# Kernel tuning notes

Measured on AMD Instinct MI355X. Metric: run time of the kernel, lower is better.

Reference implementation:

```python
import jax, jax.numpy as jnp
import numpy as np

N, E, D, L, G = 10000, 320000, 256, 5, 128
RWSE, DEG_V = 16, 1001
BN_EPS = 1e-5


def setup_inputs() -> dict:
    key = jax.random.key(0)
    ks = jax.random.split(key, 12)
    s = 1.0 / np.sqrt(D)
    return {
        'feat_id': jax.random.randint(ks[0], (N,), 0, 100000, dtype=jnp.int64 if jax.config.jax_enable_x64 else jnp.int32),
        'edge_index': jax.random.randint(ks[1], (2, E), 0, N),
        'batch_idx': jnp.sort(jax.random.randint(ks[2], (N,), 0, G)),
        'rwse': jax.random.normal(ks[3], (N, RWSE), jnp.float32),
        'in_degrees': jax.random.randint(ks[4], (N,), 0, DEG_V),
        # value_projection: Linear(fixed_input_dim=D -> D); stored as [in, out]
        'w_val': jax.random.normal(ks[5], (D, D), jnp.float32) * s,
        'b_val': jnp.zeros((D,), jnp.float32),
        # rwse_projection: Linear(RWSE -> D)
        'w_rwse': jax.random.normal(ks[6], (RWSE, D), jnp.float32) * (1.0 / np.sqrt(RWSE)),
        'b_rwse': jnp.zeros((D,), jnp.float32),
        # degree_embedding table (clamped to [0, 1000])
        'deg_emb': jax.random.normal(ks[7], (DEG_V, D), jnp.float32) * 0.02,
        # per-layer GIN MLP: Linear-ReLU-Linear, stacked over L layers
        'mlp_w1': jax.random.normal(ks[8], (L, D, D), jnp.float32) * s,
        'mlp_b1': jnp.zeros((L, D), jnp.float32),
        'mlp_w2': jax.random.normal(ks[9], (L, D, D), jnp.float32) * s,
        'mlp_b2': jnp.zeros((L, D), jnp.float32),
        # BatchNorm1d (eval mode: running stats)
        'bn_gamma': jnp.ones((L, D), jnp.float32),
        'bn_beta': jnp.zeros((L, D), jnp.float32),
        'bn_mean': jnp.zeros((L, D), jnp.float32),
        'bn_var': jax.random.uniform(ks[10], (L, D), jnp.float32, 0.5, 1.5),
        # GIN eps per layer
        'eps_gin': jnp.zeros((L,), jnp.float32),
    }


def reference(feat_id, edge_index, batch_idx, rwse, in_degrees,
              w_val, b_val, w_rwse, b_rwse, deg_emb,
              mlp_w1, mlp_b1, mlp_w2, mlp_b2,
              bn_gamma, bn_beta, bn_mean, bn_var, eps_gin):
    # --- node feature embedding ---
    h_id = jnp.remainder(feat_id, D)
    h_one = jax.nn.one_hot(h_id, D, dtype=jnp.float32)            # [N, D]
    h = h_one @ w_val + b_val + rwse @ w_rwse + b_rwse            # value + rwse projections
    deg = jnp.clip(in_degrees, 0, 1000)
    h = h + deg_emb[deg]                                          # degree embedding

    src, dst = edge_index[0], edge_index[1]
    for l in range(L):
        # GIN message passing: sum neighbor features into dst (gather -> scatter-add)
        agg = jax.ops.segment_sum(h[src], dst, num_segments=N)    # [N, D]
        y = agg + (1.0 + eps_gin[l]) * h
        # MLP (Linear-ReLU-Linear)
        y = jax.nn.relu(y @ mlp_w1[l] + mlp_b1[l]) @ mlp_w2[l] + mlp_b2[l]
        # BatchNorm1d (eval: running stats) + ReLU
        y = (y - bn_mean[l]) * (bn_gamma[l] * jax.lax.rsqrt(bn_var[l] + BN_EPS)) + bn_beta[l]
        h = jax.nn.relu(y)

    # --- mean pooling per graph ---
    sums = jax.ops.segment_sum(h, batch_idx, num_segments=G)                     # [G, D]
    cnt = jax.ops.segment_sum(jnp.ones((N, 1), h.dtype), batch_idx, num_segments=G)
    graph_feature = sums / jnp.maximum(cnt, 1.0)
    return graph_feature, h
```

## Files before the change

### kernel.cpp

```cpp
#include <hip/hip_runtime.h>
#include <hip/hip_bf16.h>

#define N_NODES 10000
#define N_EDGES 320000
#define DIM     256
#define HDIM    128
#define N_LAYERS 5
#define N_GRAPHS 128
#define RWSE_K  16

typedef __bf16 bf16_t;
typedef bf16_t bf16x8 __attribute__((ext_vector_type(8)));
typedef float  f32x4  __attribute__((ext_vector_type(4)));

__device__ inline ushort f2bf(float f) {
    union { float f; unsigned u; } v; v.f = f;
    unsigned r = v.u + 0x7fff + ((v.u >> 16) & 1);
    return (ushort)(r >> 16);
}
__device__ inline float bfbits2f(unsigned hi16) {
    union { unsigned u; float f; } v; v.u = hi16;
    return v.f;
}

__global__ __launch_bounds__(256)
void setup_kernel(const int* __restrict__ feat_id,
                  const float* __restrict__ rwse,
                  const int* __restrict__ in_deg,
                  const float* __restrict__ w_val,
                  const float* __restrict__ b_val,
                  const float* __restrict__ w_rwse,
                  const float* __restrict__ b_rwse,
                  const float* __restrict__ deg_emb,
                  ushort* __restrict__ hb_lo, ushort* __restrict__ hb_hi,
                  const int* __restrict__ ei, int* __restrict__ cnt_arr,
                  const float* __restrict__ w1, const float* __restrict__ w2,
                  ushort* __restrict__ wt1, ushort* __restrict__ wt2,
                  const float* __restrict__ gamma, const float* __restrict__ beta,
                  const float* __restrict__ mean, const float* __restrict__ var,
                  const float* __restrict__ b2, float* __restrict__ scale,
                  float* __restrict__ shift) {
    __shared__ float r[RWSE_K];
    __shared__ float t[32][33];
    int b = blockIdx.x;
    int tid = threadIdx.x;
    if (b < N_NODES) {
        int i = b, d = tid;
        if (d < RWSE_K) r[d] = rwse[i * RWSE_K + d];
        __syncthreads();
        int hid = feat_id[i] & (DIM - 1);
        int dg = in_deg[i];
        dg = dg < 0 ? 0 : (dg > 1000 ? 1000 : dg);
        float v = w_val[hid * DIM + d] + b_val[d] + b_rwse[d] + deg_emb[dg * DIM + d];
#pragma unroll
        for (int k = 0; k < RWSE_K; ++k) v += r[k] * w_rwse[k * DIM + d];
        int hh = d >> 7, dl = d & (HDIM - 1);
        (hh ? hb_hi : hb_lo)[i * HDIM + dl] = f2bf(v);
    } else if (b < 11250) {
        int e = (b - N_NODES) * 256 + tid;
        if (e < N_EDGES) atomicAdd(&cnt_arr[ei[N_EDGES + e]], 1);
    } else if (b < 11890) {
        int w_id = b - 11250;
        int l = w_id >> 7;
        int rem = w_id & 127;
        int mat = rem >> 6;
        int tile = rem & 63;
        const float* W  = (mat ? w2  : w1)  + (size_t)l * DIM * DIM;
        ushort*      Wt = (mat ? wt2 : wt1) + (size_t)l * DIM * DIM;
        int k0 = (tile >> 3) * 32, n0 = (tile & 7) * 32;
        int tx = tid & 31, ty = tid >> 5;
#pragma unroll
        for (int j = 0; j < 4; ++j)
            t[ty + j * 8][tx] = W[(k0 + ty + j * 8) * DIM + n0 + tx];
        __syncthreads();
#pragma unroll
        for (int j = 0; j < 4; ++j)
            Wt[(n0 + ty + j * 8) * DIM + k0 + tx] = f2bf(t[tx][ty + j * 8]);
    } else {
        int l = b - 11890;
        int idx = l * DIM + tid;
        float s = gamma[idx] * rsqrtf(var[idx] + 1e-5f);
        scale[idx] = s;
        shift[idx] = beta[idx] + (b2[idx] - mean[idx]) * s;
    }
}

__global__ __launch_bounds__(1024)
void scan_kernel(const int* __restrict__ cnt_arr, int* __restrict__ cur, int n) {
    __shared__ int wsum[16];
    __shared__ int carry_sh;
    int tid = threadIdx.x, wave = tid >> 6, lane = tid & 63;
    if (tid == 0) carry_sh = 0;
    __syncthreads();
    for (int base = 0; base < n; base += 1024) {
        int idx = base + tid;
        int v = (idx < n) ? cnt_arr[idx] : 0;
        int s = v;
#pragma unroll
        for (int off = 1; off < 64; off <<= 1) {
            int t = __shfl_up(s, off, 64);
            if (lane >= off) s += t;
        }
        if (lane == 63) wsum[wave] = s;
        __syncthreads();
        if (wave == 0) {
            int ws = (lane < 16) ? wsum[lane] : 0;
#pragma unroll
            for (int off = 1; off < 16; off <<= 1) {
                int t = __shfl_up(ws, off, 64);
                if (lane >= off) ws += t;
            }
            if (lane < 16) wsum[lane] = ws;
        }
        __syncthreads();
        int excl = s - v + (wave ? wsum[wave - 1] : 0) + carry_sh;
        if (idx < n) cur[idx] = excl;
        __syncthreads();
        if (tid == 0) carry_sh += wsum[15];
        __syncthreads();
    }
}

__global__ __launch_bounds__(256)
void fill_kernel(const int* __restrict__ ei, int* __restrict__ cur,
                 int* __restrict__ cs) {
    int e = blockIdx.x * 256 + threadIdx.x;
    if (e < N_EDGES) {
        int d = ei[N_EDGES + e];
        int p = atomicAdd(&cur[d], 1);
        cs[p] = ei[e];
    }
}

#define ACCV(v)                                                        \
    acc[0] += bfbits2f((v).x << 16); acc[1] += bfbits2f((v).x & 0xffff0000u); \
    acc[2] += bfbits2f((v).y << 16); acc[3] += bfbits2f((v).y & 0xffff0000u); \
    acc[4] += bfbits2f((v).z << 16); acc[5] += bfbits2f((v).z & 0xffff0000u); \
    acc[6] += bfbits2f((v).w << 16); acc[7] += bfbits2f((v).w & 0xffff0000u);

__global__ __launch_bounds__(256)
void agg_kernel(const ushort* __restrict__ hbH,
                const int* __restrict__ cur, const int* __restrict__ cs,
                const float* __restrict__ eps_gin, int layer, int hh,
                ushort* __restrict__ y) {
    int wave = threadIdx.x >> 6;
    int lane = threadIdx.x & 63;
    int quarter = lane >> 4;
    int sl = lane & 15;
    int i = blockIdx.x * 4 + wave;
    if (i >= N_NODES) return;
    const uint4* hb4 = (const uint4*)hbH;
    float acc[8];
#pragma unroll
    for (int t = 0; t < 8; ++t) acc[t] = 0.f;

    int e0 = i ? cur[i - 1] : 0;
    int e1 = cur[i];
    for (int base = e0; base < e1; base += 64) {
        int rem = e1 - base;
        int cnt = rem < 64 ? rem : 64;
        int idx = (base + lane < e1) ? cs[base + lane] : 0;
        int j = 0;
        for (; j + 8 <= cnt; j += 8) {
            int s0 = __shfl(idx, j + quarter, 64);
            int s1 = __shfl(idx, j + 4 + quarter, 64);
            uint4 v0 = hb4[(size_t)s0 * 16 + sl];
            uint4 v1 = hb4[(size_t)s1 * 16 + sl];
            ACCV(v0); ACCV(v1);
        }
        for (; j + 4 <= cnt; j += 4) {
            int s = __shfl(idx, j + quarter, 64);
            uint4 v = hb4[(size_t)s * 16 + sl];
            ACCV(v);
        }
        for (; j < cnt; ++j) {
            int s = __shfl(idx, j, 64);
            if (quarter == 0) {
                uint4 v = hb4[(size_t)s * 16 + sl];
                ACCV(v);
            }
        }
    }
#pragma unroll
    for (int t = 0; t < 8; ++t) acc[t] += __shfl_xor(acc[t], 16, 64);
#pragma unroll
    for (int t = 0; t < 8; ++t) acc[t] += __shfl_xor(acc[t], 32, 64);
    if (quarter == 0) {
        float sc = 1.0f + eps_gin[layer];
        uint4 sv = hb4[(size_t)i * 16 + sl];
        acc[0] += bfbits2f(sv.x << 16) * sc; acc[1] += bfbits2f(sv.x & 0xffff0000u) * sc;
        acc[2] += bfbits2f(sv.y << 16) * sc; acc[3] += bfbits2f(sv.y & 0xffff0000u) * sc;
        acc[4] += bfbits2f(sv.z << 16) * sc; acc[5] += bfbits2f(sv.z & 0xffff0000u) * sc;
        acc[6] += bfbits2f(sv.w << 16) * sc; acc[7] += bfbits2f(sv.w & 0xffff0000u) * sc;
        uint4 o;
        o.x = (uint)f2bf(acc[0]) | ((uint)f2bf(acc[1]) << 16);
        o.y = (uint)f2bf(acc[2]) | ((uint)f2bf(acc[3]) << 16);
        o.z = (uint)f2bf(acc[4]) | ((uint)f2bf(acc[5]) << 16);
        o.w = (uint)f2bf(acc[6]) | ((uint)f2bf(acc[7]) << 16);
        ((uint4*)y)[(size_t)i * 32 + hh * 16 + sl] = o;
    }
}

#define GBM 32

__global__ __launch_bounds__(256)
void gemm12_kernel(const ushort* __restrict__ A, const ushort* __restrict__ Wt1,
                   const float* __restrict__ b1, const ushort* __restrict__ Wt2,
                   const float* __restrict__ bnsc, const float* __restrict__ bnsh,
                   float* __restrict__ outF, ushort* __restrict__ hbl,
                   ushort* __restrict__ hbh, int nrows) {
    __shared__ __align__(16) ushort As[GBM][40];
    __shared__ __align__(16) ushort Bs[DIM][40];
    __shared__ __align__(16) ushort Ts[GBM][DIM + 8];
    int tx = threadIdx.x;
    int row0 = blockIdx.x * GBM;
    int wave = tx >> 6, lane = tx & 63, quad = lane >> 4, l16 = lane & 15;
    int wr = (wave >> 1) * 16;
    int wc = (wave & 1) * 128;
    int srow = tx >> 2;
    int skol = (tx & 3) * 8;

    f32x4 acc[8];
#pragma unroll
    for (int t = 0; t < 8; ++t) acc[t] = (f32x4){0.f, 0.f, 0.f, 0.f};

    for (int k0 = 0; k0 < DIM; k0 += 32) {
        if (tx < 128) {
            int arow = row0 + srow;
            uint4 av = make_uint4(0u, 0u, 0u, 0u);
            if (arow < nrows) av = *(const uint4*)&A[(size_t)arow * DIM + k0 + skol];
            *(uint4*)&As[srow][skol] = av;
        }
#pragma unroll
        for (int j = 0; j < 4; ++j) {
            int r = srow + 64 * j;
            *(uint4*)&Bs[r][skol] = *(const uint4*)&Wt1[(size_t)r * DIM + k0 + skol];
        }
        __syncthreads();
        bf16x8 af = *(const bf16x8*)&As[wr + l16][quad * 8];
#pragma unroll
        for (int tj = 0; tj < 8; ++tj) {
            bf16x8 bf = *(const bf16x8*)&Bs[wc + tj * 16 + l16][quad * 8];
            acc[tj] = __builtin_amdgcn_mfma_f32_16x16x32_bf16(af, bf, acc[tj], 0, 0, 0);
        }
        __syncthreads();
    }
#pragma unroll
    for (int tj = 0; tj < 8; ++tj) {
        int col = wc + tj * 16 + l16;
        float bias = b1[col];
#pragma unroll
        for (int r = 0; r < 4; ++r) {
            int rl = wr + quad * 4 + r;
            Ts[rl][col] = f2bf(fmaxf(acc[tj][r] + bias, 0.f));
        }
    }
    __syncthreads();

#pragma unroll
    for (int t = 0; t < 8; ++t) acc[t] = (f32x4){0.f, 0.f, 0.f, 0.f};
    for (int k0 = 0; k0 < DIM; k0 += 32) {
#pragma unroll
        for (int j = 0; j < 4; ++j) {
            int r = srow + 64 * j;
            *(uint4*)&Bs[r][skol] = *(const uint4*)&Wt2[(size_t)r * DIM + k0 + skol];
        }
        __syncthreads();
        bf16x8 af = *(const bf16x8*)&Ts[wr + l16][k0 + quad * 8];
#pragma unroll
        for (int tj = 0; tj < 8; ++tj) {
            bf16x8 bf = *(const bf16x8*)&Bs[wc + tj * 16 + l16][quad * 8];
            acc[tj] = __builtin_amdgcn_mfma_f32_16x16x32_bf16(af, bf, acc[tj], 0, 0, 0);
        }
        __syncthreads();
    }
#pragma unroll
    for (int tj = 0; tj < 8; ++tj) {
        int col = wc + tj * 16 + l16;
        float s = bnsc[col], sh = bnsh[col];
#pragma unroll
        for (int r = 0; r < 4; ++r) {
            int row = row0 + wr + quad * 4 + r;
            if (row < nrows) {
                float v = fmaxf(acc[tj][r] * s + sh, 0.f);
                if (outF) outF[(size_t)row * DIM + col] = v;
                if (hbl) {
                    if (col < HDIM) hbl[(size_t)row * HDIM + col] = f2bf(v);
                    else            hbh[(size_t)row * HDIM + col - HDIM] = f2bf(v);
                }
            }
        }
    }
}

__global__ __launch_bounds__(256)
void pool_kernel(const float* __restrict__ hfin, const int* __restrict__ batch,
                 float* __restrict__ out) {
    int g = blockIdx.x;
    int d = threadIdx.x;
    int l = 0, r = N_NODES;
    while (l < r) { int m = (l + r) >> 1; if (batch[m] < g) l = m + 1; else r = m; }
    int lo = l;
    r = N_NODES;
    while (l < r) { int m = (l + r) >> 1; if (batch[m] < g + 1) l = m + 1; else r = m; }
    int hi = l;
    float a0 = 0.f, a1 = 0.f, a2 = 0.f, a3 = 0.f;
    int i = lo;
    for (; i + 4 <= hi; i += 4) {
        a0 += hfin[(size_t)i * DIM + d];
        a1 += hfin[(size_t)(i + 1) * DIM + d];
        a2 += hfin[(size_t)(i + 2) * DIM + d];
        a3 += hfin[(size_t)(i + 3) * DIM + d];
    }
    for (; i < hi; ++i) a0 += hfin[(size_t)i * DIM + d];
    float c = (float)(hi - lo);
    if (c < 1.f) c = 1.f;
    out[g * DIM + d] = ((a0 + a1) + (a2 + a3)) / c;
}

extern "C" void kernel_launch(void* const* d_in, const int* in_sizes, int n_in,
                              void* d_out, int out_size, void* d_ws, size_t ws_size,
                              hipStream_t stream) {
    const int*   feat_id  = (const int*)d_in[0];
    const int*   ei       = (const int*)d_in[1];
    const int*   batch    = (const int*)d_in[2];
    const float* rwse     = (const float*)d_in[3];
    const int*   in_deg   = (const int*)d_in[4];
    const float* w_val    = (const float*)d_in[5];
    const float* b_val    = (const float*)d_in[6];
    const float* w_rwse   = (const float*)d_in[7];
    const float* b_rwse   = (const float*)d_in[8];
    const float* deg_emb  = (const float*)d_in[9];
    const float* mlp_w1   = (const float*)d_in[10];
    const float* mlp_b1   = (const float*)d_in[11];
    const float* mlp_w2   = (const float*)d_in[12];
    const float* mlp_b2   = (const float*)d_in[13];
    const float* bn_gamma = (const float*)d_in[14];
    const float* bn_beta  = (const float*)d_in[15];
    const float* bn_mean  = (const float*)d_in[16];
    const float* bn_var   = (const float*)d_in[17];
    const float* eps_gin  = (const float*)d_in[18];

    float* out = (float*)d_out;
    float* out_h = out + N_GRAPHS * DIM;

    char* w = (char*)d_ws;
    ushort* hb_lo = (ushort*)w;
    ushort* hb_hi = hb_lo + (size_t)N_NODES * HDIM;
    ushort* y     = hb_hi + (size_t)N_NODES * HDIM;
    ushort* wt1   = y + (size_t)N_NODES * DIM;
    ushort* wt2   = wt1 + (size_t)N_LAYERS * DIM * DIM;
    int* cnt_arr  = (int*)(wt2 + (size_t)N_LAYERS * DIM * DIM);
    int* cur      = cnt_arr + N_NODES;
    int* cs       = cur + N_NODES;
    float* bnsc   = (float*)(cs + N_EDGES);
    float* bnsh   = bnsc + N_LAYERS * DIM;

    hipMemsetAsync(cnt_arr, 0, N_NODES * sizeof(int), stream);

    setup_kernel<<<11895, 256, 0, stream>>>(
        feat_id, rwse, in_deg, w_val, b_val, w_rwse, b_rwse, deg_emb,
        hb_lo, hb_hi, ei, cnt_arr, mlp_w1, mlp_w2, wt1, wt2,
        bn_gamma, bn_beta, bn_mean, bn_var, mlp_b2, bnsc, bnsh);
    scan_kernel<<<1, 1024, 0, stream>>>(cnt_arr, cur, N_NODES);
    fill_kernel<<<(N_EDGES + 255) / 256, 256, 0, stream>>>(ei, cur, cs);

    int agrid = (N_NODES + 3) / 4;
    int ggrid = (N_NODES + GBM - 1) / GBM;
    for (int l = 0; l < N_LAYERS; ++l) {
        agg_kernel<<<agrid, 256, 0, stream>>>(hb_lo, cur, cs, eps_gin, l, 0, y);
        agg_kernel<<<agrid, 256, 0, stream>>>(hb_hi, cur, cs, eps_gin, l, 1, y);
        bool last = (l == N_LAYERS - 1);
        gemm12_kernel<<<ggrid, 256, 0, stream>>>(
            y, wt1 + (size_t)l * DIM * DIM, mlp_b1 + l * DIM,
            wt2 + (size_t)l * DIM * DIM, bnsc + l * DIM, bnsh + l * DIM,
            last ? out_h : nullptr,
            last ? nullptr : hb_lo, last ? nullptr : hb_hi, N_NODES);
    }

    pool_kernel<<<N_GRAPHS, 256, 0, stream>>>(out_h, batch, out);
}
```

Before: 382.1 us.

## Fuse neighbor aggregation into the per-layer MLP GEMM kernel with ping-pong buffers

Merges the two half-width aggregation kernels and the two-GEMM MLP kernel into one layer kernel per layer. Each block gathers and sums neighbor rows for its 32 nodes straight into shared memory, then runs both GEMMs from there. The node features change from split low/high halves to full-width bf16 rows, with ping-pong input/output buffers. This removes the intermediate y write and read and two launches per layer, but the gather now runs on only 313 blocks, which may limit the memory parallelism available for the random-access aggregation.

```diff
diff --git a/kernel.cpp b/kernel.cpp
--- a/kernel.cpp
+++ b/kernel.cpp
@@ -4,10 +4,10 @@
 #define N_NODES 10000
 #define N_EDGES 320000
 #define DIM     256
-#define HDIM    128
 #define N_LAYERS 5
 #define N_GRAPHS 128
 #define RWSE_K  16
+#define GBM 32
 
 typedef __bf16 bf16_t;
 typedef bf16_t bf16x8 __attribute__((ext_vector_type(8)));
@@ -32,7 +32,7 @@
                   const float* __restrict__ w_rwse,
                   const float* __restrict__ b_rwse,
                   const float* __restrict__ deg_emb,
-                  ushort* __restrict__ hb_lo, ushort* __restrict__ hb_hi,
+                  ushort* __restrict__ hb,
                   const int* __restrict__ ei, int* __restrict__ cnt_arr,
                   const float* __restrict__ w1, const float* __restrict__ w2,
                   ushort* __restrict__ wt1, ushort* __restrict__ wt2,
@@ -54,8 +54,7 @@
         float v = w_val[hid * DIM + d] + b_val[d] + b_rwse[d] + deg_emb[dg * DIM + d];
 #pragma unroll
         for (int k = 0; k < RWSE_K; ++k) v += r[k] * w_rwse[k * DIM + d];
-        int hh = d >> 7, dl = d & (HDIM - 1);
-        (hh ? hb_hi : hb_lo)[i * HDIM + dl] = f2bf(v);
+        hb[i * DIM + d] = f2bf(v);
     } else if (b < 11250) {
         int e = (b - N_NODES) * 256 + tid;
         if (e < N_EDGES) atomicAdd(&cnt_arr[ei[N_EDGES + e]], 1);
@@ -139,109 +138,97 @@
     acc[6] += bfbits2f((v).w << 16); acc[7] += bfbits2f((v).w & 0xffff0000u);
 
 __global__ __launch_bounds__(256)
-void agg_kernel(const ushort* __restrict__ hbH,
-                const int* __restrict__ cur, const int* __restrict__ cs,
-                const float* __restrict__ eps_gin, int layer, int hh,
-                ushort* __restrict__ y) {
-    int wave = threadIdx.x >> 6;
-    int lane = threadIdx.x & 63;
-    int quarter = lane >> 4;
-    int sl = lane & 15;
-    int i = blockIdx.x * 4 + wave;
-    if (i >= N_NODES) return;
-    const uint4* hb4 = (const uint4*)hbH;
-    float acc[8];
-#pragma unroll
-    for (int t = 0; t < 8; ++t) acc[t] = 0.f;
-
-    int e0 = i ? cur[i - 1] : 0;
-    int e1 = cur[i];
-    for (int base = e0; base < e1; base += 64) {
-        int rem = e1 - base;
-        int cnt = rem < 64 ? rem : 64;
-        int idx = (base + lane < e1) ? cs[base + lane] : 0;
-        int j = 0;
-        for (; j + 8 <= cnt; j += 8) {
-            int s0 = __shfl(idx, j + quarter, 64);
-            int s1 = __shfl(idx, j + 4 + quarter, 64);
-            uint4 v0 = hb4[(size_t)s0 * 16 + sl];
-            uint4 v1 = hb4[(size_t)s1 * 16 + sl];
-            ACCV(v0); ACCV(v1);
-        }
-        for (; j + 4 <= cnt; j += 4) {
-            int s = __shfl(idx, j + quarter, 64);
-            uint4 v = hb4[(size_t)s * 16 + sl];
-            ACCV(v);
-        }
-        for (; j < cnt; ++j) {
-            int s = __shfl(idx, j, 64);
-            if (quarter == 0) {
-                uint4 v = hb4[(size_t)s * 16 + sl];
-                ACCV(v);
-            }
-        }
-    }
-#pragma unroll
-    for (int t = 0; t < 8; ++t) acc[t] += __shfl_xor(acc[t], 16, 64);
-#pragma unroll
-    for (int t = 0; t < 8; ++t) acc[t] += __shfl_xor(acc[t], 32, 64);
-    if (quarter == 0) {
-        float sc = 1.0f + eps_gin[layer];
-        uint4 sv = hb4[(size_t)i * 16 + sl];
-        acc[0] += bfbits2f(sv.x << 16) * sc; acc[1] += bfbits2f(sv.x & 0xffff0000u) * sc;
-        acc[2] += bfbits2f(sv.y << 16) * sc; acc[3] += bfbits2f(sv.y & 0xffff0000u) * sc;
-        acc[4] += bfbits2f(sv.z << 16) * sc; acc[5] += bfbits2f(sv.z & 0xffff0000u) * sc;
-        acc[6] += bfbits2f(sv.w << 16) * sc; acc[7] += bfbits2f(sv.w & 0xffff0000u) * sc;
-        uint4 o;
-        o.x = (uint)f2bf(acc[0]) | ((uint)f2bf(acc[1]) << 16);
-        o.y = (uint)f2bf(acc[2]) | ((uint)f2bf(acc[3]) << 16);
-        o.z = (uint)f2bf(acc[4]) | ((uint)f2bf(acc[5]) << 16);
-        o.w = (uint)f2bf(acc[6]) | ((uint)f2bf(acc[7]) << 16);
-        ((uint4*)y)[(size_t)i * 32 + hh * 16 + sl] = o;
-    }
-}
-
-#define GBM 32
-
-__global__ __launch_bounds__(256)
-void gemm12_kernel(const ushort* __restrict__ A, const ushort* __restrict__ Wt1,
-                   const float* __restrict__ b1, const ushort* __restrict__ Wt2,
-                   const float* __restrict__ bnsc, const float* __restrict__ bnsh,
-                   float* __restrict__ outF, ushort* __restrict__ hbl,
-                   ushort* __restrict__ hbh, int nrows) {
-    __shared__ __align__(16) ushort As[GBM][40];
+void layer_kernel(const ushort* __restrict__ hb_in, ushort* __restrict__ hb_out,
+                  float* __restrict__ outF,
+                  const int* __restrict__ cur, const int* __restrict__ cs,
+                  const float* __restrict__ eps_gin, int layer,
+                  const ushort* __restrict__ Wt1, const float* __restrict__ b1,
+                  const ushort* __restrict__ Wt2,
+                  const float* __restrict__ bnsc, const float* __restrict__ bnsh,
+                  int nrows) {
+    __shared__ __align__(16) ushort AT[GBM][DIM + 8];
     __shared__ __align__(16) ushort Bs[DIM][40];
-    __shared__ __align__(16) ushort Ts[GBM][DIM + 8];
     int tx = threadIdx.x;
     int row0 = blockIdx.x * GBM;
-    int wave = tx >> 6, lane = tx & 63, quad = lane >> 4, l16 = lane & 15;
+    int wave = tx >> 6, lane = tx & 63, half = lane >> 5, sl = lane & 31;
+    int quad = lane >> 4, l16 = lane & 15;
+    const uint4* hb4 = (const uint4*)hb_in;
+    float sc = 1.0f + eps_gin[layer];
+
+    for (int j = 0; j < 8; ++j) {
+        int i = row0 + wave * 8 + j;
+        if (i >= nrows) break;
+        float acc[8];
+#pragma unroll
+        for (int t = 0; t < 8; ++t) acc[t] = 0.f;
+        int e0 = i ? cur[i - 1] : 0;
+        int e1 = cur[i];
+        for (int base = e0; base < e1; base += 64) {
+            int rem = e1 - base;
+            int cnt = rem < 64 ? rem : 64;
+            int idx = (base + lane < e1) ? cs[base + lane] : 0;
+            int jj = 0;
+            for (; jj + 8 <= cnt; jj += 8) {
+                int s0 = __shfl(idx, jj + half, 64);
+                int s1 = __shfl(idx, jj + 2 + half, 64);
+                int s2 = __shfl(idx, jj + 4 + half, 64);
+                int s3 = __shfl(idx, jj + 6 + half, 64);
+                uint4 v0 = hb4[(size_t)s0 * 32 + sl];
+                uint4 v1 = hb4[(size_t)s1 * 32 + sl];
+                uint4 v2 = hb4[(size_t)s2 * 32 + sl];
+                uint4 v3 = hb4[(size_t)s3 * 32 + sl];
+                ACCV(v0); ACCV(v1); ACCV(v2); ACCV(v3);
+            }
+            for (; jj + 2 <= cnt; jj += 2) {
+                int s = __shfl(idx, jj + half, 64);
+                uint4 v = hb4[(size_t)s * 32 + sl];
+                ACCV(v);
+            }
+            if (jj < cnt) {
+                int s = __shfl(idx, jj, 64);
+                if (half == 0) {
+                    uint4 v = hb4[(size_t)s * 32 + sl];
+                    ACCV(v);
+                }
+            }
+        }
+#pragma unroll
+        for (int t = 0; t < 8; ++t) acc[t] += __shfl_xor(acc[t], 32, 64);
+        if (half == 0) {
+            uint4 sv = hb4[(size_t)i * 32 + sl];
+            acc[0] += bfbits2f(sv.x << 16) * sc; acc[1] += bfbits2f(sv.x & 0xffff0000u) * sc;
+            acc[2] += bfbits2f(sv.y << 16) * sc; acc[3] += bfbits2f(sv.y & 0xffff0000u) * sc;
+            acc[4] += bfbits2f(sv.z << 16) * sc; acc[5] += bfbits2f(sv.z & 0xffff0000u) * sc;
+            acc[6] += bfbits2f(sv.w << 16) * sc; acc[7] += bfbits2f(sv.w & 0xffff0000u) * sc;
+            uint4 o;
+            o.x = (uint)f2bf(acc[0]) | ((uint)f2bf(acc[1]) << 16);
+            o.y = (uint)f2bf(acc[2]) | ((uint)f2bf(acc[3]) << 16);
+            o.z = (uint)f2bf(acc[4]) | ((uint)f2bf(acc[5]) << 16);
+            o.w = (uint)f2bf(acc[6]) | ((uint)f2bf(acc[7]) << 16);
+            *(uint4*)&AT[wave * 8 + j][sl * 8] = o;
+        }
+    }
+    __syncthreads();
+
     int wr = (wave >> 1) * 16;
     int wc = (wave & 1) * 128;
     int srow = tx >> 2;
     int skol = (tx & 3) * 8;
-
-    f32x4 acc[8];
-#pragma unroll
-    for (int t = 0; t < 8; ++t) acc[t] = (f32x4){0.f, 0.f, 0.f, 0.f};
-
+    f32x4 acc4[8];
+#pragma unroll
+    for (int t = 0; t < 8; ++t) acc4[t] = (f32x4){0.f, 0.f, 0.f, 0.f};
     for (int k0 = 0; k0 < DIM; k0 += 32) {
-        if (tx < 128) {
-            int arow = row0 + srow;
-            uint4 av = make_uint4(0u, 0u, 0u, 0u);
-            if (arow < nrows) av = *(const uint4*)&A[(size_t)arow * DIM + k0 + skol];
-            *(uint4*)&As[srow][skol] = av;
-        }
-#pragma unroll
-        for (int j = 0; j < 4; ++j) {
-            int r = srow + 64 * j;
+#pragma unroll
+        for (int jj = 0; jj < 4; ++jj) {
+            int r = srow + 64 * jj;
             *(uint4*)&Bs[r][skol] = *(const uint4*)&Wt1[(size_t)r * DIM + k0 + skol];
         }
         __syncthreads();
-        bf16x8 af = *(const bf16x8*)&As[wr + l16][quad * 8];
+        bf16x8 af = *(const bf16x8*)&AT[wr + l16][k0 + quad * 8];
 #pragma unroll
         for (int tj = 0; tj < 8; ++tj) {
             bf16x8 bf = *(const bf16x8*)&Bs[wc + tj * 16 + l16][quad * 8];
-            acc[tj] = __builtin_amdgcn_mfma_f32_16x16x32_bf16(af, bf, acc[tj], 0, 0, 0);
+            acc4[tj] = __builtin_amdgcn_mfma_f32_16x16x32_bf16(af, bf, acc4[tj], 0, 0, 0);
         }
         __syncthreads();
     }
@@ -250,27 +237,25 @@
         int col = wc + tj * 16 + l16;
         float bias = b1[col];
 #pragma unroll
-        for (int r = 0; r < 4; ++r) {
-            int rl = wr + quad * 4 + r;
-            Ts[rl][col] = f2bf(fmaxf(acc[tj][r] + bias, 0.f));
-        }
+        for (int r = 0; r < 4; ++r)
+            AT[wr + quad * 4 + r][col] = f2bf(fmaxf(acc4[tj][r] + bias, 0.f));
     }
     __syncthreads();
 
 #pragma unroll
-    for (int t = 0; t < 8; ++t) acc[t] = (f32x4){0.f, 0.f, 0.f, 0.f};
+    for (int t = 0; t < 8; ++t) acc4[t] = (f32x4){0.f, 0.f, 0.f, 0.f};
     for (int k0 = 0; k0 < DIM; k0 += 32) {
 #pragma unroll
-        for (int j = 0; j < 4; ++j) {
-            int r = srow + 64 * j;
+        for (int jj = 0; jj < 4; ++jj) {
+            int r = srow + 64 * jj;
             *(uint4*)&Bs[r][skol] = *(const uint4*)&Wt2[(size_t)r * DIM + k0 + skol];
         }
         __syncthreads();
-        bf16x8 af = *(const bf16x8*)&Ts[wr + l16][k0 + quad * 8];
+        bf16x8 af = *(const bf16x8*)&AT[wr + l16][k0 + quad * 8];
 #pragma unroll
         for (int tj = 0; tj < 8; ++tj) {
             bf16x8 bf = *(const bf16x8*)&Bs[wc + tj * 16 + l16][quad * 8];
-            acc[tj] = __builtin_amdgcn_mfma_f32_16x16x32_bf16(af, bf, acc[tj], 0, 0, 0);
+            acc4[tj] = __builtin_amdgcn_mfma_f32_16x16x32_bf16(af, bf, acc4[tj], 0, 0, 0);
         }
         __syncthreads();
     }
@@ -282,12 +267,9 @@
         for (int r = 0; r < 4; ++r) {
             int row = row0 + wr + quad * 4 + r;
             if (row < nrows) {
-                float v = fmaxf(acc[tj][r] * s + sh, 0.f);
+                float v = fmaxf(acc4[tj][r] * s + sh, 0.f);
                 if (outF) outF[(size_t)row * DIM + col] = v;
-                if (hbl) {
-                    if (col < HDIM) hbl[(size_t)row * HDIM + col] = f2bf(v);
-                    else            hbh[(size_t)row * HDIM + col - HDIM] = f2bf(v);
-                }
+                if (hb_out) hb_out[(size_t)row * DIM + col] = f2bf(v);
             }
         }
     }
@@ -345,37 +327,37 @@
     float* out_h = out + N_GRAPHS * DIM;
 
     char* w = (char*)d_ws;
-    ushort* hb_lo = (ushort*)w;
-    ushort* hb_hi = hb_lo + (size_t)N_NODES * HDIM;
-    ushort* y     = hb_hi + (size_t)N_NODES * HDIM;
-    ushort* wt1   = y + (size_t)N_NODES * DIM;
-    ushort* wt2   = wt1 + (size_t)N_LAYERS * DIM * DIM;
-    int* cnt_arr  = (int*)(wt2 + (size_t)N_LAYERS * DIM * DIM);
-    int* cur      = cnt_arr + N_NODES;
-    int* cs       = cur + N_NODES;
-    float* bnsc   = (float*)(cs + N_EDGES);
-    float* bnsh   = bnsc + N_LAYERS * DIM;
+    ushort* hbA  = (ushort*)w;
+    ushort* hbB  = hbA + (size_t)N_NODES * DIM;
+    ushort* wt1  = hbB + (size_t)N_NODES * DIM;
+    ushort* wt2  = wt1 + (size_t)N_LAYERS * DIM * DIM;
+    int* cnt_arr = (int*)(wt2 + (size_t)N_LAYERS * DIM * DIM);
+    int* cur     = cnt_arr + N_NODES;
+    int* cs      = cur + N_NODES;
+    float* bnsc  = (float*)(cs + N_EDGES);
+    float* bnsh  = bnsc + N_LAYERS * DIM;
 
     hipMemsetAsync(cnt_arr, 0, N_NODES * sizeof(int), stream);
 
     setup_kernel<<<11895, 256, 0, stream>>>(
         feat_id, rwse, in_deg, w_val, b_val, w_rwse, b_rwse, deg_emb,
-        hb_lo, hb_hi, ei, cnt_arr, mlp_w1, mlp_w2, wt1, wt2,
+        hbA, ei, cnt_arr, mlp_w1, mlp_w2, wt1, wt2,
         bn_gamma, bn_beta, bn_mean, bn_var, mlp_b2, bnsc, bnsh);
     scan_kernel<<<1, 1024, 0, stream>>>(cnt_arr, cur, N_NODES);
     fill_kernel<<<(N_EDGES + 255) / 256, 256, 0, stream>>>(ei, cur, cs);
 
-    int agrid = (N_NODES + 3) / 4;
     int ggrid = (N_NODES + GBM - 1) / GBM;
+    ushort* hin = hbA;
+    ushort* hout = hbB;
     for (int l = 0; l < N_LAYERS; ++l) {
-        agg_kernel<<<agrid, 256, 0, stream>>>(hb_lo, cur, cs, eps_gin, l, 0, y);
-        agg_kernel<<<agrid, 256, 0, stream>>>(hb_hi, cur, cs, eps_gin, l, 1, y);
         bool last = (l == N_LAYERS - 1);
-        gemm12_kernel<<<ggrid, 256, 0, stream>>>(
-            y, wt1 + (size_t)l * DIM * DIM, mlp_b1 + l * DIM,
-            wt2 + (size_t)l * DIM * DIM, bnsc + l * DIM, bnsh + l * DIM,
-            last ? out_h : nullptr,
-            last ? nullptr : hb_lo, last ? nullptr : hb_hi, N_NODES);
+        layer_kernel<<<ggrid, 256, 0, stream>>>(
+            hin, last ? nullptr : hout, last ? out_h : nullptr,
+            cur, cs, eps_gin, l,
+            wt1 + (size_t)l * DIM * DIM, mlp_b1 + l * DIM,
+            wt2 + (size_t)l * DIM * DIM,
+            bnsc + l * DIM, bnsh + l * DIM, N_NODES);
+        ushort* tmp = hin; hin = hout; hout = tmp;
     }
 
     pool_kernel<<<N_GRAPHS, 256, 0, stream>>>(out_h, batch, out);
```

Result: slower. 411.8 us (+7.8%).
